# Kernel optimization log

Hardware: AMD Instinct MI355X
Metric: run time of the kernel (lower is better)

## Reference

```python
import jax, jax.numpy as jnp
import numpy as np

B, S, F, DK = 4, 2048, 1024, 1024

def setup_inputs() -> dict:
    key = jax.random.key(0)
    ks = jax.random.split(key, 9)
    sF = 1.0 / np.sqrt(F)
    sD = 1.0 / np.sqrt(DK)
    return {
        "x":  jax.random.normal(ks[0], (B, S, F), dtype=jnp.float32),
        "Wq": jax.random.normal(ks[1], (DK, F), dtype=jnp.float32) * sF,
        "bq": jax.random.normal(ks[2], (DK,), dtype=jnp.float32) * sF,
        "Wk": jax.random.normal(ks[3], (DK, F), dtype=jnp.float32) * sF,
        "bk": jax.random.normal(ks[4], (DK,), dtype=jnp.float32) * sF,
        "Wv": jax.random.normal(ks[5], (DK, F), dtype=jnp.float32) * sF,
        "bv": jax.random.normal(ks[6], (DK,), dtype=jnp.float32) * sF,
        "Wo": jax.random.normal(ks[7], (F, DK), dtype=jnp.float32) * sD,
        "bo": jax.random.normal(ks[8], (F,), dtype=jnp.float32) * sD,
    }

def reference(x, Wq, bq, Wk, bk, Wv, bv, Wo, bo):
    # Linear layers (torch convention: y = x @ W.T + b)
    q = jnp.einsum('bsf,df->bsd', x, Wq) + bq  # (B,S,DK)
    k = jnp.einsum('bsf,df->bsd', x, Wk) + bk  # (B,S,DK)
    v = jnp.einsum('bsf,df->bsd', x, Wv) + bv  # (B,S,DK)
    scale = 1.0 / (q.shape[-1] ** 0.5)
    scores = jnp.einsum('bqd,bkd->bqk', q, k) * scale  # (B,Sq,Sk)
    # Faithful to original: softmax over dim=-2 (the QUERY axis)
    attn = jax.nn.softmax(scores, axis=-2)
    ctx = jnp.einsum('bqk,bkd->bqd', attn, v)  # (B,S,DK)
    out = jnp.einsum('bsd,fd->bsf', ctx, Wo) + bo  # (B,S,F)
    return out
```

## Files before the change

kernel.cpp:

```cpp
#include <hip/hip_runtime.h>
#include <hip/hip_bf16.h>
#include <math.h>

typedef __bf16 bf16_t;
typedef __bf16 bf16x8 __attribute__((ext_vector_type(8)));
typedef float f32x4 __attribute__((ext_vector_type(4)));


__device__ __forceinline__ void g2l16(const bf16_t* g, bf16_t* l) {
  __builtin_amdgcn_global_load_lds(
      (const __attribute__((address_space(1))) void*)g,
      (__attribute__((address_space(3))) void*)l, 16, 0, 0);
}

__device__ __forceinline__ float waveMax(float v) {
#pragma unroll
  for (int o = 32; o > 0; o >>= 1) v = fmaxf(v, __shfl_xor(v, o));
  return v;
}
__device__ __forceinline__ float waveSum(float v) {
#pragma unroll
  for (int o = 32; o > 0; o >>= 1) v += __shfl_xor(v, o);
  return v;
}

__device__ __forceinline__ bf16x8 rdf(const char* base, int row, int kbyte) {
  int off = (row << 7) + kbyte;
  off ^= (row & 7) << 4;
  return *reinterpret_cast<const bf16x8*>(base + off);
}


__global__ __launch_bounds__(256) void cast_f32_to_bf16(
    const float* __restrict__ in, bf16_t* __restrict__ out, long n) {
  long i = ((long)blockIdx.x * 256 + threadIdx.x) * 8;
  if (i >= n) return;
  float4 a = *reinterpret_cast<const float4*>(in + i);
  float4 b = *reinterpret_cast<const float4*>(in + i + 4);
  bf16x8 o;
  o[0] = (bf16_t)a.x; o[1] = (bf16_t)a.y; o[2] = (bf16_t)a.z; o[3] = (bf16_t)a.w;
  o[4] = (bf16_t)b.x; o[5] = (bf16_t)b.y; o[6] = (bf16_t)b.z; o[7] = (bf16_t)b.w;
  *reinterpret_cast<bf16x8*>(out + i) = o;
}


#define MFMA_ ____nope

#define STAGE256(d, o, h, t) do {                                              \
  const bf16_t* gsrc_ = ((o) ? Bb : Ab) + (long)((h) * 128 + srl) * K +        \
                        (long)(t) * 64 + sgsw;                                 \
  bf16_t* ldsb_ = &lds[d][o][(h) * 8192] + ldst;                               \
  g2l16(gsrc_, ldsb_);                                                         \
  g2l16(gsrc_ + 64L * K, ldsb_ + 4096);                                        \
} while (0)

#define AREAD256(d, qm) do {                                                   \
  const char* Ab_ = (const char*)&lds[d][0][0];                                \
  int r_ = (qm) * 128 + wr2 * 64 + rA;                                         \
  a0 = rdf(Ab_, r_, kb);      a1 = rdf(Ab_, r_, kb + 64);                      \
  a2 = rdf(Ab_, r_ + 16, kb); a3 = rdf(Ab_, r_ + 16, kb + 64);                 \
  a4 = rdf(Ab_, r_ + 32, kb); a5 = rdf(Ab_, r_ + 32, kb + 64);                 \
  a6 = rdf(Ab_, r_ + 48, kb); a7 = rdf(Ab_, r_ + 48, kb + 64);                 \
} while (0)

#define BREAD256(d, qn, r0v, r1v, r2v, r3v) do {                               \
  const char* Bb_ = (const char*)&lds[d][1][0];                                \
  int c_ = (qn) * 128 + wc2 * 32 + rA;                                         \
  r0v = rdf(Bb_, c_, kb);      r1v = rdf(Bb_, c_, kb + 64);                    \
  r2v = rdf(Bb_, c_ + 16, kb); r3v = rdf(Bb_, c_ + 16, kb + 64);               \
} while (0)

#define MFMA16(qm, qn, b0v, b1v, b2v, b3v) do {                                \
  acc[(qm)*4+0][(qn)*2+0] = __builtin_amdgcn_mfma_f32_16x16x32_bf16(a0, b0v, acc[(qm)*4+0][(qn)*2+0], 0,0,0); \
  acc[(qm)*4+0][(qn)*2+0] = __builtin_amdgcn_mfma_f32_16x16x32_bf16(a1, b1v, acc[(qm)*4+0][(qn)*2+0], 0,0,0); \
  acc[(qm)*4+1][(qn)*2+0] = __builtin_amdgcn_mfma_f32_16x16x32_bf16(a2, b0v, acc[(qm)*4+1][(qn)*2+0], 0,0,0); \
  acc[(qm)*4+1][(qn)*2+0] = __builtin_amdgcn_mfma_f32_16x16x32_bf16(a3, b1v, acc[(qm)*4+1][(qn)*2+0], 0,0,0); \
  acc[(qm)*4+2][(qn)*2+0] = __builtin_amdgcn_mfma_f32_16x16x32_bf16(a4, b0v, acc[(qm)*4+2][(qn)*2+0], 0,0,0); \
  acc[(qm)*4+2][(qn)*2+0] = __builtin_amdgcn_mfma_f32_16x16x32_bf16(a5, b1v, acc[(qm)*4+2][(qn)*2+0], 0,0,0); \
  acc[(qm)*4+3][(qn)*2+0] = __builtin_amdgcn_mfma_f32_16x16x32_bf16(a6, b0v, acc[(qm)*4+3][(qn)*2+0], 0,0,0); \
  acc[(qm)*4+3][(qn)*2+0] = __builtin_amdgcn_mfma_f32_16x16x32_bf16(a7, b1v, acc[(qm)*4+3][(qn)*2+0], 0,0,0); \
  acc[(qm)*4+0][(qn)*2+1] = __builtin_amdgcn_mfma_f32_16x16x32_bf16(a0, b2v, acc[(qm)*4+0][(qn)*2+1], 0,0,0); \
  acc[(qm)*4+0][(qn)*2+1] = __builtin_amdgcn_mfma_f32_16x16x32_bf16(a1, b3v, acc[(qm)*4+0][(qn)*2+1], 0,0,0); \
  acc[(qm)*4+1][(qn)*2+1] = __builtin_amdgcn_mfma_f32_16x16x32_bf16(a2, b2v, acc[(qm)*4+1][(qn)*2+1], 0,0,0); \
  acc[(qm)*4+1][(qn)*2+1] = __builtin_amdgcn_mfma_f32_16x16x32_bf16(a3, b3v, acc[(qm)*4+1][(qn)*2+1], 0,0,0); \
  acc[(qm)*4+2][(qn)*2+1] = __builtin_amdgcn_mfma_f32_16x16x32_bf16(a4, b2v, acc[(qm)*4+2][(qn)*2+1], 0,0,0); \
  acc[(qm)*4+2][(qn)*2+1] = __builtin_amdgcn_mfma_f32_16x16x32_bf16(a5, b3v, acc[(qm)*4+2][(qn)*2+1], 0,0,0); \
  acc[(qm)*4+3][(qn)*2+1] = __builtin_amdgcn_mfma_f32_16x16x32_bf16(a6, b2v, acc[(qm)*4+3][(qn)*2+1], 0,0,0); \
  acc[(qm)*4+3][(qn)*2+1] = __builtin_amdgcn_mfma_f32_16x16x32_bf16(a7, b3v, acc[(qm)*4+3][(qn)*2+1], 0,0,0); \
} while (0)

#define PH_ENTER() do {                                                        \
  __builtin_amdgcn_s_barrier();                                                \
  asm volatile("s_waitcnt lgkmcnt(0)" ::: "memory");                           \
  __builtin_amdgcn_sched_barrier(0);                                           \
  __builtin_amdgcn_s_setprio(1);                                               \
} while (0)

#define PH_EXIT() do {                                                         \
  __builtin_amdgcn_s_setprio(0);                                               \
  __builtin_amdgcn_s_barrier();                                                \
  __builtin_amdgcn_sched_barrier(0);                                           \
} while (0)

template <int EPI>
__launch_bounds__(512, 2)
__global__ void gemm256(const bf16_t* __restrict__ A, const bf16_t* __restrict__ B,
                        int K, float alpha,
                        void* __restrict__ C0, void* __restrict__ C1, void* __restrict__ C2,
                        const float* __restrict__ bias0, const float* __restrict__ bias1,
                        const float* __restrict__ bias2,
                        int Ncols, long sA, long sB, long sC) {
  __shared__ bf16_t lds[2][2][16384];

  const int tid = threadIdx.x;
  const int lane = tid & 63;
  const int w = tid >> 6;
  const int wr2 = w >> 2;
  const int wc2 = w & 3;
  const int rA = lane & 15;
  const int kb = (lane >> 4) << 4;

  const int bm = blockIdx.x * 256;
  const int bn = blockIdx.y * 256;
  const bf16_t* Ab = A + (long)blockIdx.z * sA + (long)bm * K;
  const bf16_t* Bb = B + (long)blockIdx.z * sB + (long)bn * K;

  const int srl = tid >> 3;
  const int sgr = tid & 7;
  const int sgsw = (sgr ^ (srl & 7)) * 8;
  const int ldst = srl * 64 + sgr * 8;

  f32x4 acc[8][4] = {};
  bf16x8 a0, a1, a2, a3, a4, a5, a6, a7;
  bf16x8 p0, p1, p2, p3, q0, q1, q2, q3;

  const int NT = K >> 6;

  STAGE256(0, 0, 0, 0); STAGE256(0, 1, 0, 0);
  STAGE256(0, 0, 1, 0); STAGE256(0, 1, 1, 0);
  STAGE256(1, 0, 0, 1); STAGE256(1, 1, 0, 1);
  asm volatile("s_waitcnt vmcnt(4)" ::: "memory");
  __builtin_amdgcn_s_barrier();
  __builtin_amdgcn_sched_barrier(0);

  int t = 0;
  for (int it = 0; it < NT / 2 - 1; ++it, t += 2) {
    AREAD256(0, 0); BREAD256(0, 0, p0, p1, p2, p3);
    STAGE256(1, 0, 1, t + 1);
    PH_ENTER(); MFMA16(0, 0, p0, p1, p2, p3); PH_EXIT();
    BREAD256(0, 1, q0, q1, q2, q3);
    STAGE256(1, 1, 1, t + 1);
    PH_ENTER(); MFMA16(0, 1, q0, q1, q2, q3); PH_EXIT();
    AREAD256(0, 1);
    STAGE256(0, 0, 0, t + 2);
    PH_ENTER(); MFMA16(1, 0, p0, p1, p2, p3); PH_EXIT();
    STAGE256(0, 1, 0, t + 2);
    asm volatile("s_waitcnt vmcnt(4)" ::: "memory");
    PH_ENTER(); MFMA16(1, 1, q0, q1, q2, q3); PH_EXIT();
    AREAD256(1, 0); BREAD256(1, 0, p0, p1, p2, p3);
    STAGE256(0, 0, 1, t + 2);
    PH_ENTER(); MFMA16(0, 0, p0, p1, p2, p3); PH_EXIT();
    BREAD256(1, 1, q0, q1, q2, q3);
    STAGE256(0, 1, 1, t + 2);
    PH_ENTER(); MFMA16(0, 1, q0, q1, q2, q3); PH_EXIT();
    AREAD256(1, 1);
    STAGE256(1, 0, 0, t + 3);
    PH_ENTER(); MFMA16(1, 0, p0, p1, p2, p3); PH_EXIT();
    STAGE256(1, 1, 0, t + 3);
    asm volatile("s_waitcnt vmcnt(4)" ::: "memory");
    PH_ENTER(); MFMA16(1, 1, q0, q1, q2, q3); PH_EXIT();
  }

  AREAD256(0, 0); BREAD256(0, 0, p0, p1, p2, p3);
  STAGE256(1, 0, 1, t + 1);
  PH_ENTER(); MFMA16(0, 0, p0, p1, p2, p3); PH_EXIT();
  BREAD256(0, 1, q0, q1, q2, q3);
  STAGE256(1, 1, 1, t + 1);
  PH_ENTER(); MFMA16(0, 1, q0, q1, q2, q3); PH_EXIT();
  AREAD256(0, 1);
  PH_ENTER(); MFMA16(1, 0, p0, p1, p2, p3); PH_EXIT();
  asm volatile("s_waitcnt vmcnt(0)" ::: "memory");
  PH_ENTER(); MFMA16(1, 1, q0, q1, q2, q3); PH_EXIT();
  AREAD256(1, 0); BREAD256(1, 0, p0, p1, p2, p3);
  PH_ENTER(); MFMA16(0, 0, p0, p1, p2, p3); PH_EXIT();
  BREAD256(1, 1, q0, q1, q2, q3);
  PH_ENTER(); MFMA16(0, 1, q0, q1, q2, q3); PH_EXIT();
  AREAD256(1, 1);
  PH_ENTER(); MFMA16(1, 0, p0, p1, p2, p3); PH_EXIT();
  PH_ENTER(); MFMA16(1, 1, q0, q1, q2, q3); PH_EXIT();

  const int rr = (lane >> 4) * 4;
  const int cc = lane & 15;
#pragma unroll
  for (int qm = 0; qm < 2; ++qm)
#pragma unroll
    for (int m = 0; m < 4; ++m) {
      const int grow = bm + qm * 128 + wr2 * 64 + m * 16 + rr;
#pragma unroll
      for (int qn = 0; qn < 2; ++qn)
#pragma unroll
        for (int n = 0; n < 2; ++n) {
          const int gcol = bn + qn * 128 + wc2 * 32 + n * 16 + cc;
          const f32x4 v = acc[qm * 4 + m][qn * 2 + n];
          if (EPI == 0) {
            float* C = (float*)C0 + (long)blockIdx.z * sC;
#pragma unroll
            for (int j = 0; j < 4; ++j)
              C[(long)(grow + j) * Ncols + gcol] = v[j] * alpha;
          } else {
            const int sel = gcol >> 10;
            const int lcol = gcol & 1023;
            const float* bp = sel == 0 ? bias0 : (sel == 1 ? bias1 : bias2);
            bf16_t* op = sel == 0 ? (bf16_t*)C0 : (sel == 1 ? (bf16_t*)C1 : (bf16_t*)C2);
            const float bv = bp[lcol];
#pragma unroll
            for (int j = 0; j < 4; ++j)
              op[(long)(grow + j) * 1024 + lcol] = (bf16_t)(v[j] + bv);
          }
        }
    }
  (void)Ncols;
}


template <int OUT_BF16, int HAS_BIAS>
__launch_bounds__(256, 2)
__global__ void gemm_bt(const bf16_t* __restrict__ A, const bf16_t* __restrict__ B,
                        const float* __restrict__ bias, void* __restrict__ Cv,
                        int M, int N, int K, float alpha,
                        long sA, long sB, long sC) {
  const bf16_t* Ab = A + (long)blockIdx.z * sA;
  const bf16_t* Bb = B + (long)blockIdx.z * sB;
  const int bm = blockIdx.x * 128;
  const int bn = blockIdx.y * 128;

  __shared__ bf16_t sAt[128 * 32];
  __shared__ bf16_t sBt[128 * 32];

  const int tid = threadIdx.x;
  const int lane = tid & 63;
  const int w = tid >> 6;
  const int wr = (w >> 1) * 64;
  const int wc = (w & 1) * 64;

  f32x4 acc[4][4] = {};

  const int r0 = tid >> 2;
  const int c0 = (tid & 3) * 8;
  const int r1 = 64 + (tid >> 2);
  const long lds0 = (long)tid * 8;
  const long lds1 = 2048 + (long)tid * 8;

  const int arow = wr + (lane & 15);
  const int brow = wc + (lane & 15);
  const int koff = (lane >> 4) * 8;

  const int nK = K >> 5;
  for (int kt = 0; kt < nK; ++kt) {
    const int k0 = kt << 5;
    g2l16(Ab + (long)(bm + r0) * K + k0 + c0, sAt + lds0);
    g2l16(Ab + (long)(bm + r1) * K + k0 + c0, sAt + lds1);
    g2l16(Bb + (long)(bn + r0) * K + k0 + c0, sBt + lds0);
    g2l16(Bb + (long)(bn + r1) * K + k0 + c0, sBt + lds1);
    __syncthreads();

    bf16x8 af[4], bfr[4];
#pragma unroll
    for (int m = 0; m < 4; ++m)
      af[m] = *reinterpret_cast<const bf16x8*>(sAt + (arow + m * 16) * 32 + koff);
#pragma unroll
    for (int n = 0; n < 4; ++n)
      bfr[n] = *reinterpret_cast<const bf16x8*>(sBt + (brow + n * 16) * 32 + koff);
#pragma unroll
    for (int m = 0; m < 4; ++m)
#pragma unroll
      for (int n = 0; n < 4; ++n)
        acc[m][n] = __builtin_amdgcn_mfma_f32_16x16x32_bf16(af[m], bfr[n], acc[m][n], 0, 0, 0);
    __syncthreads();
  }

  const int rbase = bm + wr + (lane >> 4) * 4;
  const int cbase = bn + wc + (lane & 15);
#pragma unroll
  for (int n = 0; n < 4; ++n) {
    const int col = cbase + n * 16;
    float bv = 0.f;
    if (HAS_BIAS) bv = bias[col];
#pragma unroll
    for (int m = 0; m < 4; ++m) {
      const int row0 = rbase + m * 16;
#pragma unroll
      for (int j = 0; j < 4; ++j) {
        float v = acc[m][n][j] * alpha + bv;
        if (OUT_BF16) {
          bf16_t* C = (bf16_t*)Cv + (long)blockIdx.z * sC;
          C[(long)(row0 + j) * N + col] = (bf16_t)v;
        } else {
          float* C = (float*)Cv + (long)blockIdx.z * sC;
          C[(long)(row0 + j) * N + col] = v;
        }
      }
    }
  }
}


__global__ __launch_bounds__(256) void row_stats(const float* __restrict__ S,
                                                 float* __restrict__ rmax,
                                                 float* __restrict__ rinv) {
  const long row = blockIdx.x;
  const float* p = S + row * 2048;
  const int t = threadIdx.x;
  float4 a = *reinterpret_cast<const float4*>(p + t * 8);
  float4 b = *reinterpret_cast<const float4*>(p + t * 8 + 4);
  float m = fmaxf(fmaxf(fmaxf(a.x, a.y), fmaxf(a.z, a.w)),
                  fmaxf(fmaxf(b.x, b.y), fmaxf(b.z, b.w)));
  m = waveMax(m);
  __shared__ float red[4];
  __shared__ float red2[4];
  if ((t & 63) == 0) red[t >> 6] = m;
  __syncthreads();
  m = fmaxf(fmaxf(red[0], red[1]), fmaxf(red[2], red[3]));
  float s = expf(a.x - m) + expf(a.y - m) + expf(a.z - m) + expf(a.w - m) +
            expf(b.x - m) + expf(b.y - m) + expf(b.z - m) + expf(b.w - m);
  s = waveSum(s);
  if ((t & 63) == 0) red2[t >> 6] = s;
  __syncthreads();
  s = red2[0] + red2[1] + red2[2] + red2[3];
  if (t == 0) { rmax[row] = m; rinv[row] = 1.0f / s; }
}

__global__ __launch_bounds__(256) void softmax_T(const float* __restrict__ S,
                                                 const float* __restrict__ rmax,
                                                 const float* __restrict__ rinv,
                                                 bf16_t* __restrict__ attn) {
  const int b = blockIdx.z;
  const int q0 = blockIdx.x * 64;
  const int kk0 = blockIdx.y * 64;
  __shared__ bf16_t tile[64][72];
  const int t = threadIdx.x;
  const int i = t >> 2;
  const int qj = (t & 3) * 16;
  const long grow = (long)b * 2048 + kk0 + i;
  const float mx = rmax[grow];
  const float ri = rinv[grow];
  const float* src = S + grow * 2048 + q0 + qj;
#pragma unroll
  for (int u = 0; u < 4; ++u) {
    float4 v = *reinterpret_cast<const float4*>(src + u * 4);
    tile[i][qj + u * 4 + 0] = (bf16_t)(expf(v.x - mx) * ri);
    tile[i][qj + u * 4 + 1] = (bf16_t)(expf(v.y - mx) * ri);
    tile[i][qj + u * 4 + 2] = (bf16_t)(expf(v.z - mx) * ri);
    tile[i][qj + u * 4 + 3] = (bf16_t)(expf(v.w - mx) * ri);
  }
  __syncthreads();
  const int j = t >> 2;
  const int kc = (t & 3) * 16;
  bf16x8 o0, o1;
#pragma unroll
  for (int u = 0; u < 8; ++u) o0[u] = tile[kc + u][j];
#pragma unroll
  for (int u = 0; u < 8; ++u) o1[u] = tile[kc + 8 + u][j];
  bf16_t* dst = attn + ((long)b * 2048 + q0 + j) * 2048 + kk0 + kc;
  *reinterpret_cast<bf16x8*>(dst) = o0;
  *reinterpret_cast<bf16x8*>(dst + 8) = o1;
}

__global__ __launch_bounds__(256) void transpose_bf16k(const bf16_t* __restrict__ in,
                                                       bf16_t* __restrict__ out,
                                                       int R, int C) {
  const int b = blockIdx.z;
  const int r0 = blockIdx.x * 64;
  const int c0 = blockIdx.y * 64;
  __shared__ bf16_t tile[64][72];
  const int t = threadIdx.x;
  const int i = t >> 2;
  const int cj = (t & 3) * 16;
  const bf16_t* src = in + ((long)b * R + r0 + i) * C + c0 + cj;
  bf16x8 a0 = *reinterpret_cast<const bf16x8*>(src);
  bf16x8 a1 = *reinterpret_cast<const bf16x8*>(src + 8);
#pragma unroll
  for (int u = 0; u < 8; ++u) { tile[i][cj + u] = a0[u]; tile[i][cj + 8 + u] = a1[u]; }
  __syncthreads();
  const int j = t >> 2;
  const int rc = (t & 3) * 16;
  bf16x8 o0, o1;
#pragma unroll
  for (int u = 0; u < 8; ++u) o0[u] = tile[rc + u][j];
#pragma unroll
  for (int u = 0; u < 8; ++u) o1[u] = tile[rc + 8 + u][j];
  bf16_t* dst = out + ((long)b * C + c0 + j) * R + r0 + rc;
  *reinterpret_cast<bf16x8*>(dst) = o0;
  *reinterpret_cast<bf16x8*>(dst + 8) = o1;
}


extern "C" void kernel_launch(void* const* d_in, const int* in_sizes, int n_in,
                              void* d_out, int out_size, void* d_ws, size_t ws_size,
                              hipStream_t stream) {
  const float* x  = (const float*)d_in[0];
  const float* Wq = (const float*)d_in[1];
  const float* bq = (const float*)d_in[2];
  const float* Wk = (const float*)d_in[3];
  const float* bk = (const float*)d_in[4];
  const float* Wv = (const float*)d_in[5];
  const float* bv = (const float*)d_in[6];
  const float* Wo = (const float*)d_in[7];
  const float* bo = (const float*)d_in[8];
  float* out = (float*)d_out;
  char* ws = (char*)d_ws;

  const long MB = 1024L * 1024L;
  bf16_t* xb    = (bf16_t*)(ws + 0);
  bf16_t* Wqkvb = (bf16_t*)(ws + 16 * MB);
  bf16_t* Wob   = (bf16_t*)(ws + 22 * MB);
  bf16_t* Qb    = (bf16_t*)(ws + 24 * MB);
  bf16_t* Kb    = (bf16_t*)(ws + 40 * MB);
  bf16_t* Vb    = (bf16_t*)(ws + 56 * MB);
  float*  ST    = (float*)(ws + 72 * MB);
  bf16_t* attn  = (bf16_t*)(ws + 136 * MB);
  float*  rmax  = (float*)(ws + 168 * MB);
  float*  rinv  = (float*)(ws + 168 * MB + 32768);
  bf16_t* VT    = (bf16_t*)(ws + 0);
  bf16_t* ctxb  = (bf16_t*)(ws + 24 * MB);

  cast_f32_to_bf16<<<4096, 256, 0, stream>>>(x, xb, 8388608);
  cast_f32_to_bf16<<<512, 256, 0, stream>>>(Wq, Wqkvb, 1048576);
  cast_f32_to_bf16<<<512, 256, 0, stream>>>(Wk, Wqkvb + 1048576, 1048576);
  cast_f32_to_bf16<<<512, 256, 0, stream>>>(Wv, Wqkvb + 2097152, 1048576);
  cast_f32_to_bf16<<<512, 256, 0, stream>>>(Wo, Wob, 1048576);

  gemm256<1><<<dim3(32, 12, 1), 512, 0, stream>>>(
      xb, Wqkvb, 1024, 1.0f, Qb, Kb, Vb, bq, bk, bv, 3072, 0, 0, 0);

  gemm256<0><<<dim3(8, 8, 4), 512, 0, stream>>>(
      Kb, Qb, 1024, 0.03125f, ST, nullptr, nullptr, nullptr, nullptr, nullptr,
      2048, 2048L * 1024, 2048L * 1024, 2048L * 2048);

  row_stats<<<8192, 256, 0, stream>>>(ST, rmax, rinv);
  dim3 gsm(32, 32, 4);
  softmax_T<<<gsm, 256, 0, stream>>>(ST, rmax, rinv, attn);

  dim3 gtr(32, 16, 4);
  transpose_bf16k<<<gtr, 256, 0, stream>>>(Vb, VT, 2048, 1024);

  dim3 gctx(16, 8, 4);
  gemm_bt<1, 0><<<gctx, 256, 0, stream>>>(attn, VT, nullptr, ctxb, 2048, 1024, 2048, 1.0f,
                                          2048L * 2048, 1024L * 2048, 2048L * 1024);

  dim3 gout(64, 8, 1);
  gemm_bt<0, 1><<<gout, 256, 0, stream>>>(ctxb, Wob, bo, out, 8192, 1024, 1024, 1.0f, 0, 0, 0);

  (void)in_sizes; (void)n_in; (void)out_size; (void)ws_size;
}
```

Before: 335.0 us.

## Fuse exp into score GEMM epilogue, write bf16 probabilities, add XCD swizzle

The score GEMM now applies exp to the scaled scores in its epilogue and stores bf16 instead of fp32. That halves the intermediate traffic and removes the separate max/exp passes; a lighter row-sum kernel and a scale-and-transpose kernel finish the softmax. Block indices in both GEMM kernels are remapped with an XCD-aware swizzle for better cache locality, and the four weight casts are merged into one launch. Dropping the max subtraction risks overflow or precision loss when scores are large, so it relies on the scores being well bounded.

```diff
diff --git a/kernel.cpp b/kernel.cpp
--- a/kernel.cpp
+++ b/kernel.cpp
@@ -13,15 +13,19 @@
       (__attribute__((address_space(3))) void*)l, 16, 0, 0);
 }
 
-__device__ __forceinline__ float waveMax(float v) {
-#pragma unroll
-  for (int o = 32; o > 0; o >>= 1) v = fmaxf(v, __shfl_xor(v, o));
-  return v;
-}
 __device__ __forceinline__ float waveSum(float v) {
 #pragma unroll
   for (int o = 32; o > 0; o >>= 1) v += __shfl_xor(v, o);
   return v;
+}
+
+__device__ __forceinline__ void xcdswz(int& bx, int& by, int& bz) {
+  const int gx = gridDim.x, gy = gridDim.y;
+  const int n = gx * gy * gridDim.z;
+  int f = bx + gx * (by + gy * bz);
+  const int cpx = n >> 3;
+  int s = (f & 7) * cpx + (f >> 3);
+  bx = s % gx; s /= gx; by = s % gy; bz = s / gy;
 }
 
 __device__ __forceinline__ bf16x8 rdf(const char* base, int row, int kbyte) {
@@ -43,8 +47,24 @@
   *reinterpret_cast<bf16x8*>(out + i) = o;
 }
 
-
-#define MFMA_ ____nope
+__global__ __launch_bounds__(256) void cast_w4(
+    const float* __restrict__ w0, const float* __restrict__ w1,
+    const float* __restrict__ w2, const float* __restrict__ w3,
+    bf16_t* __restrict__ o0, bf16_t* __restrict__ o1,
+    bf16_t* __restrict__ o2, bf16_t* __restrict__ o3) {
+  const int sel = blockIdx.x >> 9;
+  const int blk = blockIdx.x & 511;
+  const float* in = sel == 0 ? w0 : (sel == 1 ? w1 : (sel == 2 ? w2 : w3));
+  bf16_t* out = sel == 0 ? o0 : (sel == 1 ? o1 : (sel == 2 ? o2 : o3));
+  long i = ((long)blk * 256 + threadIdx.x) * 8;
+  float4 a = *reinterpret_cast<const float4*>(in + i);
+  float4 b = *reinterpret_cast<const float4*>(in + i + 4);
+  bf16x8 o;
+  o[0] = (bf16_t)a.x; o[1] = (bf16_t)a.y; o[2] = (bf16_t)a.z; o[3] = (bf16_t)a.w;
+  o[4] = (bf16_t)b.x; o[5] = (bf16_t)b.y; o[6] = (bf16_t)b.z; o[7] = (bf16_t)b.w;
+  *reinterpret_cast<bf16x8*>(out + i) = o;
+}
+
 
 #define STAGE256(d, o, h, t) do {                                              \
   const bf16_t* gsrc_ = ((o) ? Bb : Ab) + (long)((h) * 128 + srl) * K +        \
@@ -112,6 +132,9 @@
                         int Ncols, long sA, long sB, long sC) {
   __shared__ bf16_t lds[2][2][16384];
 
+  int bx = blockIdx.x, by = blockIdx.y, bz = blockIdx.z;
+  xcdswz(bx, by, bz);
+
   const int tid = threadIdx.x;
   const int lane = tid & 63;
   const int w = tid >> 6;
@@ -120,10 +143,10 @@
   const int rA = lane & 15;
   const int kb = (lane >> 4) << 4;
 
-  const int bm = blockIdx.x * 256;
-  const int bn = blockIdx.y * 256;
-  const bf16_t* Ab = A + (long)blockIdx.z * sA + (long)bm * K;
-  const bf16_t* Bb = B + (long)blockIdx.z * sB + (long)bn * K;
+  const int bm = bx * 256;
+  const int bn = by * 256;
+  const bf16_t* Ab = A + (long)bz * sA + (long)bm * K;
+  const bf16_t* Bb = B + (long)bz * sB + (long)bn * K;
 
   const int srl = tid >> 3;
   const int sgr = tid & 7;
@@ -202,12 +225,7 @@
         for (int n = 0; n < 2; ++n) {
           const int gcol = bn + qn * 128 + wc2 * 32 + n * 16 + cc;
           const f32x4 v = acc[qm * 4 + m][qn * 2 + n];
-          if (EPI == 0) {
-            float* C = (float*)C0 + (long)blockIdx.z * sC;
-#pragma unroll
-            for (int j = 0; j < 4; ++j)
-              C[(long)(grow + j) * Ncols + gcol] = v[j] * alpha;
-          } else {
+          if (EPI == 1) {
             const int sel = gcol >> 10;
             const int lcol = gcol & 1023;
             const float* bp = sel == 0 ? bias0 : (sel == 1 ? bias1 : bias2);
@@ -216,6 +234,11 @@
 #pragma unroll
             for (int j = 0; j < 4; ++j)
               op[(long)(grow + j) * 1024 + lcol] = (bf16_t)(v[j] + bv);
+          } else {
+            bf16_t* C = (bf16_t*)C0 + (long)bz * sC;
+#pragma unroll
+            for (int j = 0; j < 4; ++j)
+              C[(long)(grow + j) * Ncols + gcol] = (bf16_t)__expf(v[j] * alpha);
           }
         }
     }
@@ -229,10 +252,12 @@
                         const float* __restrict__ bias, void* __restrict__ Cv,
                         int M, int N, int K, float alpha,
                         long sA, long sB, long sC) {
-  const bf16_t* Ab = A + (long)blockIdx.z * sA;
-  const bf16_t* Bb = B + (long)blockIdx.z * sB;
-  const int bm = blockIdx.x * 128;
-  const int bn = blockIdx.y * 128;
+  int bxi = blockIdx.x, byi = blockIdx.y, bzi = blockIdx.z;
+  xcdswz(bxi, byi, bzi);
+  const bf16_t* Ab = A + (long)bzi * sA;
+  const bf16_t* Bb = B + (long)bzi * sB;
+  const int bm = bxi * 128;
+  const int bn = byi * 128;
 
   __shared__ bf16_t sAt[128 * 32];
   __shared__ bf16_t sBt[128 * 32];
@@ -293,10 +318,10 @@
       for (int j = 0; j < 4; ++j) {
         float v = acc[m][n][j] * alpha + bv;
         if (OUT_BF16) {
-          bf16_t* C = (bf16_t*)Cv + (long)blockIdx.z * sC;
+          bf16_t* C = (bf16_t*)Cv + (long)bzi * sC;
           C[(long)(row0 + j) * N + col] = (bf16_t)v;
         } else {
-          float* C = (float*)Cv + (long)blockIdx.z * sC;
+          float* C = (float*)Cv + (long)bzi * sC;
           C[(long)(row0 + j) * N + col] = v;
         }
       }
@@ -305,35 +330,27 @@
 }
 
 
-__global__ __launch_bounds__(256) void row_stats(const float* __restrict__ S,
-                                                 float* __restrict__ rmax,
-                                                 float* __restrict__ rinv) {
+__global__ __launch_bounds__(256) void row_sums(const bf16_t* __restrict__ P,
+                                                float* __restrict__ rinv) {
   const long row = blockIdx.x;
-  const float* p = S + row * 2048;
+  const bf16_t* p = P + row * 2048;
   const int t = threadIdx.x;
-  float4 a = *reinterpret_cast<const float4*>(p + t * 8);
-  float4 b = *reinterpret_cast<const float4*>(p + t * 8 + 4);
-  float m = fmaxf(fmaxf(fmaxf(a.x, a.y), fmaxf(a.z, a.w)),
-                  fmaxf(fmaxf(b.x, b.y), fmaxf(b.z, b.w)));
-  m = waveMax(m);
+  bf16x8 a = *reinterpret_cast<const bf16x8*>(p + t * 8);
+  float s = 0.f;
+#pragma unroll
+  for (int u = 0; u < 8; ++u) s += (float)a[u];
+  s = waveSum(s);
   __shared__ float red[4];
-  __shared__ float red2[4];
-  if ((t & 63) == 0) red[t >> 6] = m;
+  if ((t & 63) == 0) red[t >> 6] = s;
   __syncthreads();
-  m = fmaxf(fmaxf(red[0], red[1]), fmaxf(red[2], red[3]));
-  float s = expf(a.x - m) + expf(a.y - m) + expf(a.z - m) + expf(a.w - m) +
-            expf(b.x - m) + expf(b.y - m) + expf(b.z - m) + expf(b.w - m);
-  s = waveSum(s);
-  if ((t & 63) == 0) red2[t >> 6] = s;
-  __syncthreads();
-  s = red2[0] + red2[1] + red2[2] + red2[3];
-  if (t == 0) { rmax[row] = m; rinv[row] = 1.0f / s; }
-}
-
-__global__ __launch_bounds__(256) void softmax_T(const float* __restrict__ S,
-                                                 const float* __restrict__ rmax,
-                                                 const float* __restrict__ rinv,
-                                                 bf16_t* __restrict__ attn) {
+  s = red[0] + red[1] + red[2] + red[3];
+  if (t == 0) rinv[row] = 1.0f / s;
+}
+
+
+__global__ __launch_bounds__(256) void scale_T(const bf16_t* __restrict__ P,
+                                               const float* __restrict__ rinv,
+                                               bf16_t* __restrict__ attn) {
   const int b = blockIdx.z;
   const int q0 = blockIdx.x * 64;
   const int kk0 = blockIdx.y * 64;
@@ -342,16 +359,14 @@
   const int i = t >> 2;
   const int qj = (t & 3) * 16;
   const long grow = (long)b * 2048 + kk0 + i;
-  const float mx = rmax[grow];
   const float ri = rinv[grow];
-  const float* src = S + grow * 2048 + q0 + qj;
-#pragma unroll
-  for (int u = 0; u < 4; ++u) {
-    float4 v = *reinterpret_cast<const float4*>(src + u * 4);
-    tile[i][qj + u * 4 + 0] = (bf16_t)(expf(v.x - mx) * ri);
-    tile[i][qj + u * 4 + 1] = (bf16_t)(expf(v.y - mx) * ri);
-    tile[i][qj + u * 4 + 2] = (bf16_t)(expf(v.z - mx) * ri);
-    tile[i][qj + u * 4 + 3] = (bf16_t)(expf(v.w - mx) * ri);
+  const bf16_t* src = P + grow * 2048 + q0 + qj;
+  bf16x8 v0 = *reinterpret_cast<const bf16x8*>(src);
+  bf16x8 v1 = *reinterpret_cast<const bf16x8*>(src + 8);
+#pragma unroll
+  for (int u = 0; u < 8; ++u) {
+    tile[i][qj + u] = (bf16_t)((float)v0[u] * ri);
+    tile[i][qj + 8 + u] = (bf16_t)((float)v1[u] * ri);
   }
   __syncthreads();
   const int j = t >> 2;
@@ -365,6 +380,7 @@
   *reinterpret_cast<bf16x8*>(dst) = o0;
   *reinterpret_cast<bf16x8*>(dst + 8) = o1;
 }
+
 
 __global__ __launch_bounds__(256) void transpose_bf16k(const bf16_t* __restrict__ in,
                                                        bf16_t* __restrict__ out,
@@ -417,29 +433,26 @@
   bf16_t* Qb    = (bf16_t*)(ws + 24 * MB);
   bf16_t* Kb    = (bf16_t*)(ws + 40 * MB);
   bf16_t* Vb    = (bf16_t*)(ws + 56 * MB);
-  float*  ST    = (float*)(ws + 72 * MB);
+  bf16_t* Pp    = (bf16_t*)(ws + 72 * MB);
   bf16_t* attn  = (bf16_t*)(ws + 136 * MB);
-  float*  rmax  = (float*)(ws + 168 * MB);
-  float*  rinv  = (float*)(ws + 168 * MB + 32768);
+  float*  rinv  = (float*)(ws + 168 * MB);
   bf16_t* VT    = (bf16_t*)(ws + 0);
   bf16_t* ctxb  = (bf16_t*)(ws + 24 * MB);
 
   cast_f32_to_bf16<<<4096, 256, 0, stream>>>(x, xb, 8388608);
-  cast_f32_to_bf16<<<512, 256, 0, stream>>>(Wq, Wqkvb, 1048576);
-  cast_f32_to_bf16<<<512, 256, 0, stream>>>(Wk, Wqkvb + 1048576, 1048576);
-  cast_f32_to_bf16<<<512, 256, 0, stream>>>(Wv, Wqkvb + 2097152, 1048576);
-  cast_f32_to_bf16<<<512, 256, 0, stream>>>(Wo, Wob, 1048576);
+  cast_w4<<<2048, 256, 0, stream>>>(Wq, Wk, Wv, Wo,
+                                    Wqkvb, Wqkvb + 1048576, Wqkvb + 2097152, Wob);
 
   gemm256<1><<<dim3(32, 12, 1), 512, 0, stream>>>(
       xb, Wqkvb, 1024, 1.0f, Qb, Kb, Vb, bq, bk, bv, 3072, 0, 0, 0);
 
-  gemm256<0><<<dim3(8, 8, 4), 512, 0, stream>>>(
-      Kb, Qb, 1024, 0.03125f, ST, nullptr, nullptr, nullptr, nullptr, nullptr,
+  gemm256<2><<<dim3(8, 8, 4), 512, 0, stream>>>(
+      Kb, Qb, 1024, 0.03125f, Pp, nullptr, nullptr, nullptr, nullptr, nullptr,
       2048, 2048L * 1024, 2048L * 1024, 2048L * 2048);
 
-  row_stats<<<8192, 256, 0, stream>>>(ST, rmax, rinv);
+  row_sums<<<8192, 256, 0, stream>>>(Pp, rinv);
   dim3 gsm(32, 32, 4);
-  softmax_T<<<gsm, 256, 0, stream>>>(ST, rmax, rinv, attn);
+  scale_T<<<gsm, 256, 0, stream>>>(Pp, rinv, attn);
 
   dim3 gtr(32, 16, 4);
   transpose_bf16k<<<gtr, 256, 0, stream>>>(Vb, VT, 2048, 1024);
```

New measurement: 312.8 us. 1.07x faster.
